# Kernel optimization log

Measured on AMD Instinct MI355X. Metric: run time of the kernel, lower is better.

The kernel has to match this reference:

```python
import jax, jax.numpy as jnp
import numpy as np

DILATION = 6
KS = 3
N = KS * KS  # 9 kernel sample points
PAD = 1      # zero padding inside DeformConv2d
EPS = 1e-5


def conv2d(x, w, b=None, padding=0):
    out = jax.lax.conv_general_dilated(
        x, w, window_strides=(1, 1),
        padding=[(padding, padding), (padding, padding)],
        dimension_numbers=('NCHW', 'OIHW', 'NCHW'))
    if b is not None:
        out = out + b[None, :, None, None]
    return out


def batchnorm_train(x, gamma, beta):
    # training-mode BN (module default): batch statistics over (N,H,W)
    mean = x.mean(axis=(0, 2, 3), keepdims=True)
    var = x.var(axis=(0, 2, 3), keepdims=True)
    return gamma[None, :, None, None] * (x - mean) * jax.lax.rsqrt(var + EPS) + beta[None, :, None, None]


def deform_conv(x, p_w, p_b, m_w, m_b, d_w, d_b, w):
    b, c, h, wd = x.shape
    offset = conv2d(x, p_w, p_b, padding=1)                 # (b, 2N, h, w)
    m = jax.nn.sigmoid(conv2d(x, m_w, m_b, padding=1))      # (b, N, h, w) modulation
    s = 2.0 * jax.nn.sigmoid(conv2d(x, d_w, d_b, padding=1))  # (b,1,h,w) adaptive dilation scale (=1 at logit 0)
    xp = jnp.pad(x, ((0, 0), (0, 0), (PAD, PAD), (PAD, PAD)))
    Hp, Wp = h + 2 * PAD, wd + 2 * PAD
    # kernel grid p_n, row-major (kh, kw) to match conv weight layout
    rng = jnp.arange(-(KS - 1) // 2, (KS - 1) // 2 + 1, dtype=x.dtype)
    pn_x, pn_y = jnp.meshgrid(rng, rng, indexing='ij')
    pn_x, pn_y = pn_x.reshape(-1), pn_y.reshape(-1)          # (N,)
    # base sampling positions (offset by PAD into padded map)
    p0_x = jnp.arange(1, h + 1, dtype=x.dtype)[:, None, None]    # (h,1,1)
    p0_y = jnp.arange(1, wd + 1, dtype=x.dtype)[None, :, None]   # (1,w,1)
    off = offset.transpose(0, 2, 3, 1)   # (b,h,w,2N)
    s_ = s.transpose(0, 2, 3, 1)         # (b,h,w,1)
    px = p0_x + DILATION * s_ * pn_x + off[..., :N]   # (b,h,w,N)
    py = p0_y + DILATION * s_ * pn_y + off[..., N:]
    fx, fy = jnp.floor(px), jnp.floor(py)
    qx_lt = jnp.clip(fx, 0, Hp - 1).astype(jnp.int32)
    qy_lt = jnp.clip(fy, 0, Wp - 1).astype(jnp.int32)
    qx_rb = jnp.clip(fx + 1, 0, Hp - 1).astype(jnp.int32)
    qy_rb = jnp.clip(fy + 1, 0, Wp - 1).astype(jnp.int32)
    pxc = jnp.clip(px, 0, Hp - 1)
    pyc = jnp.clip(py, 0, Wp - 1)
    g_lt = (1 + (qx_lt - pxc)) * (1 + (qy_lt - pyc))
    g_rb = (1 - (qx_rb - pxc)) * (1 - (qy_rb - pyc))
    g_lb = (1 + (qx_lt - pxc)) * (1 - (qy_rb - pyc))
    g_rt = (1 - (qx_rb - pxc)) * (1 + (qy_lt - pyc))

    def gather(qx, qy):
        idx = (qx * Wp + qy).reshape(b, 1, -1)                    # (b,1,h*w*N)
        xf = xp.reshape(b, c, Hp * Wp)
        out = jnp.take_along_axis(xf, jnp.broadcast_to(idx, (b, c, idx.shape[-1])), axis=2)
        return out.reshape(b, c, h, wd, N)

    x_off = (g_lt[:, None] * gather(qx_lt, qy_lt)
             + g_rb[:, None] * gather(qx_rb, qy_rb)
             + g_lb[:, None] * gather(qx_lt, qy_rb)
             + g_rt[:, None] * gather(qx_rb, qy_lt))
    x_off = x_off * m.transpose(0, 2, 3, 1)[:, None]              # modulation
    # final 3x3 conv over gathered samples == contraction over (c, N)
    return jnp.einsum('bchwn,ocn->bohw', x_off, w.reshape(w.shape[0], c, N))


def setup_inputs() -> dict:
    key = jax.random.key(0)
    ks = jax.random.split(key, 12)
    cin, c1, c2 = 512, 256, 64
    b, h, w = 2, 96, 96
    def rn(k, shape, scale):
        return jax.random.normal(k, shape, dtype=jnp.float32) * scale
    return {
        'x': rn(ks[0], (b, cin, h, w), 1.0),
        'bn1_g': jnp.ones((cin,), jnp.float32),
        'bn1_b': jnp.zeros((cin,), jnp.float32),
        'conv1_w': rn(ks[1], (c1, cin, 1, 1), (1.0 / cin) ** 0.5),
        'conv1_b': jnp.zeros((c1,), jnp.float32),
        'bn2_g': jnp.ones((c1,), jnp.float32),
        'bn2_b': jnp.zeros((c1,), jnp.float32),
        'p_w': rn(ks[2], (2 * N, c1, 3, 3), 0.01),
        'p_b': jnp.zeros((2 * N,), jnp.float32),
        'm_w': rn(ks[3], (N, c1, 3, 3), 0.01),
        'm_b': jnp.zeros((N,), jnp.float32),
        'd_w': rn(ks[4], (1, c1, 3, 3), 0.01),
        'd_b': jnp.zeros((1,), jnp.float32),
        'dconv_w': rn(ks[5], (c2, c1, 3, 3), (1.0 / (c1 * 9)) ** 0.5),
    }


def reference(x, bn1_g, bn1_b, conv1_w, conv1_b, bn2_g, bn2_b,
              p_w, p_b, m_w, m_b, d_w, d_b, dconv_w):
    f = jax.nn.relu(batchnorm_train(x, bn1_g, bn1_b))
    f = conv2d(f, conv1_w, conv1_b)
    f = batchnorm_train(f, bn2_g, bn2_b)
    return deform_conv(f, p_w, p_b, m_w, m_b, d_w, d_b, dconv_w)
```

## Files before the change

kernel.cpp:

```cpp
#include <hip/hip_runtime.h>
#include <hip/hip_bf16.h>
#include <math.h>

#define BATCH 2
#define CIN 512
#define C1 256
#define C2 64
#define HH 96
#define WW 96
#define HWSZ 9216
#define NPIX 18432
#define HP 98
#define WP 98

typedef __attribute__((ext_vector_type(8))) short bf16x8;
typedef __attribute__((ext_vector_type(4))) short bf16x4;
typedef __attribute__((ext_vector_type(4))) float f32x4;
typedef __attribute__((ext_vector_type(4))) unsigned int u32x4;
typedef __attribute__((ext_vector_type(2))) unsigned int u32x2;
typedef unsigned short u16;
typedef unsigned int u32;

__device__ __forceinline__ float bfu2f(u16 u) {
  u32 v = ((u32)u) << 16; return __builtin_bit_cast(float, v);
}
__device__ __forceinline__ u16 f2bfu(float f) {
  return __builtin_bit_cast(u16, __float2bfloat16(f));
}
__device__ __forceinline__ float rd_any(const void* p, size_t i, int fl) {
  return fl ? bfu2f(((const u16*)p)[i]) : ((const float*)p)[i];
}
__device__ __forceinline__ int get_fl(const u32* g1raw) {
  return g1raw[0] != 0x3F800000u;
}
__device__ __forceinline__ bf16x8 lds_frag(const u16* p) {
  bf16x4 lo = *(const bf16x4*)p;
  bf16x4 hi = *(const bf16x4*)(p + 4);
  bf16x8 r;
  r[0] = lo[0]; r[1] = lo[1]; r[2] = lo[2]; r[3] = lo[3];
  r[4] = hi[0]; r[5] = hi[1]; r[6] = hi[2]; r[7] = hi[3];
  return r;
}
__device__ __forceinline__ void split4(const f32x4& v, u32x2& ph, u32x2& pl) {
  u16 h0 = f2bfu(v[0]), h1 = f2bfu(v[1]), h2 = f2bfu(v[2]), h3 = f2bfu(v[3]);
  u16 l0 = f2bfu(v[0] - bfu2f(h0)), l1 = f2bfu(v[1] - bfu2f(h1));
  u16 l2 = f2bfu(v[2] - bfu2f(h2)), l3 = f2bfu(v[3] - bfu2f(h3));
  ph = (u32x2){(u32)h0 | ((u32)h1 << 16), (u32)h2 | ((u32)h3 << 16)};
  pl = (u32x2){(u32)l0 | ((u32)l1 << 16), (u32)l2 | ((u32)l3 << 16)};
}

__global__ __launch_bounds__(256) void prep_kernel(
    const void* cw, const void* pw, const void* mw, const void* dw, const void* dcw,
    const void* cb, const void* g1, const void* b1, const void* g2, const void* b2,
    const void* pb, const void* mb, const void* db,
    u16* __restrict__ W1b, u16* __restrict__ W1l,
    u16* __restrict__ Wofa, u16* __restrict__ Wofal,
    u16* __restrict__ Wab, u16* __restrict__ Wabl,
    float* __restrict__ canon, float* __restrict__ statz) {
  int e = blockIdx.x * 256 + threadIdx.x;
  if (e >= 356380) return;
  int fl = get_fl((const u32*)g1);
  if (e < 131072) {
    float v = rd_any(cw, e, fl);
    u16 h = f2bfu(v);
    W1b[e] = h; W1l[e] = f2bfu(v - bfu2f(h));
  } else if (e < 204800) {
    int i = e - 131072;
    int tap = i >> 13; int r = i & 8191; int m = r >> 8; int c = r & 255;
    float v = 0.f;
    if (m < 18)       v = rd_any(pw, (size_t)(m * 256 + c) * 9 + tap, fl);
    else if (m < 27)  v = rd_any(mw, (size_t)((m - 18) * 256 + c) * 9 + tap, fl);
    else if (m == 27) v = rd_any(dw, (size_t)c * 9 + tap, fl);
    u16 h = f2bfu(v);
    Wofa[i] = h; Wofal[i] = f2bfu(v - bfu2f(h));
  } else if (e < 352256) {
    int i = e - 204800;
    int n = i >> 14; int r = i & 16383; int o = r >> 8; int c = r & 255;
    float v = rd_any(dcw, (size_t)(o * 256 + c) * 9 + n, fl);
    u16 h = f2bfu(v);
    Wab[i] = h; Wabl[i] = f2bfu(v - bfu2f(h));
  } else if (e < 354076) {
    int i = e - 352256;
    const void* src; int off;
    if      (i < 256)  { src = cb; off = i; }
    else if (i < 768)  { src = g1; off = i - 256; }
    else if (i < 1280) { src = b1; off = i - 768; }
    else if (i < 1536) { src = g2; off = i - 1280; }
    else if (i < 1792) { src = b2; off = i - 1536; }
    else if (i < 1810) { src = pb; off = i - 1792; }
    else if (i < 1819) { src = mb; off = i - 1810; }
    else               { src = db; off = i - 1819; }
    canon[i] = rd_any(src, off, fl);
  } else {
    statz[e - 354076] = 0.f;
  }
}

__global__ __launch_bounds__(256) void bn_stats_kernel(
    const void* __restrict__ x, const float* __restrict__ gamma,
    const float* __restrict__ beta, float* __restrict__ scale,
    float* __restrict__ shift, float* __restrict__ sums, float* __restrict__ sumsq,
    int* __restrict__ cnt, const u32* __restrict__ g1raw, int force, int C) {
  int c = blockIdx.x, part = blockIdx.y, tid = threadIdx.x;
  int fl = force ? 1 : get_fl(g1raw);
  int b = part >> 1, half = part & 1;
  size_t base = ((size_t)(b * C + c)) * HWSZ + half * (HWSZ / 2);
  float s = 0.f, q = 0.f;
  if (fl) {
    const u16* p = (const u16*)x + base;
    for (int i = tid; i < 576; i += 256) {
      u32x4 U = *(const u32x4*)(p + i * 8);
      #pragma unroll
      for (int k = 0; k < 4; ++k) {
        float v0 = bfu2f((u16)(U[k] & 0xffff));
        float v1 = bfu2f((u16)(U[k] >> 16));
        s += v0 + v1; q = fmaf(v0, v0, fmaf(v1, v1, q));
      }
    }
  } else {
    const float* p = (const float*)x + base;
    for (int i = tid; i < 1152; i += 256) {
      f32x4 v = *(const f32x4*)(p + i * 4);
      #pragma unroll
      for (int k = 0; k < 4; ++k) { s += v[k]; q = fmaf(v[k], v[k], q); }
    }
  }
  __shared__ float sh[512];
  sh[tid] = s; sh[tid + 256] = q;
  __syncthreads();
  for (int off = 128; off > 0; off >>= 1) {
    if (tid < off) { sh[tid] += sh[tid + off]; sh[tid + 256] += sh[tid + 256 + off]; }
    __syncthreads();
  }
  if (tid == 0) {
    atomicAdd(&sums[c], sh[0]);
    atomicAdd(&sumsq[c], sh[256]);
    __threadfence();
    int old = atomicAdd(&cnt[c], 1);
    if (old == 3) {
      float S = atomicAdd(&sums[c], 0.f);
      float Q = atomicAdd(&sumsq[c], 0.f);
      float mean = S * (1.f / (float)NPIX);
      float var  = fmaxf(Q * (1.f / (float)NPIX) - mean * mean, 0.f);
      float sc = gamma[c] * rsqrtf(var + 1e-5f);
      scale[c] = sc;
      shift[c] = beta[c] - mean * sc;
    }
  }
}

__global__ __launch_bounds__(256) void conv1x1_kernel(
    const void* __restrict__ x, const u16* __restrict__ W1b, const u16* __restrict__ W1l,
    const float* __restrict__ cb, const float* __restrict__ scale,
    const float* __restrict__ shift, const u32* __restrict__ g1raw,
    u16* __restrict__ f1) {
  __shared__ u16 Bh[64][68];
  __shared__ u16 Bl[64][68];
  int tid = threadIdx.x;
  int fl = get_fl(g1raw);
  int bxr = blockIdx.x;
  int bx = (bxr & 7) * 36 + (bxr >> 3);
  int p0 = bx * 64;
  int co0 = blockIdx.y * 128;
  int b = p0 / HWSZ;
  int hw0 = p0 % HWSZ;
  int lane = tid & 63, wv = tid >> 6, quad = lane >> 4, mr = lane & 15;
  int m0 = co0 + wv * 32;
  f32x4 acc[2][4];
  #pragma unroll
  for (int i = 0; i < 2; ++i)
    #pragma unroll
    for (int j = 0; j < 4; ++j) acc[i][j] = (f32x4){0.f, 0.f, 0.f, 0.f};

  int spx = tid & 63, cg = tid >> 6;
  int gpx = hw0 + spx;
  for (int c0 = 0; c0 < CIN; c0 += 64) {
    __syncthreads();
    #pragma unroll
    for (int j = 0; j < 8; ++j) {
      int ci = c0 + cg * 16 + j * 2;
      float v0, v1;
      if (fl) {
        const u16* xb = (const u16*)x;
        v0 = bfu2f(xb[((size_t)(b * CIN + ci)) * HWSZ + gpx]);
        v1 = bfu2f(xb[((size_t)(b * CIN + ci + 1)) * HWSZ + gpx]);
      } else {
        const float* xf = (const float*)x;
        v0 = xf[((size_t)(b * CIN + ci)) * HWSZ + gpx];
        v1 = xf[((size_t)(b * CIN + ci + 1)) * HWSZ + gpx];
      }
      v0 = fmaxf(fmaf(v0, scale[ci], shift[ci]), 0.f);
      v1 = fmaxf(fmaf(v1, scale[ci + 1], shift[ci + 1]), 0.f);
      u16 h0 = f2bfu(v0), h1 = f2bfu(v1);
      u16 l0 = f2bfu(v0 - bfu2f(h0)), l1 = f2bfu(v1 - bfu2f(h1));
      *(u32*)&Bh[spx][cg * 16 + j * 2] = (u32)h0 | ((u32)h1 << 16);
      *(u32*)&Bl[spx][cg * 16 + j * 2] = (u32)l0 | ((u32)l1 << 16);
    }
    __syncthreads();
    #pragma unroll
    for (int kk2 = 0; kk2 < 2; ++kk2) {
      int kk = kk2 * 32;
      #pragma unroll
      for (int mf = 0; mf < 2; ++mf) {
        size_t wix = (size_t)(m0 + mf * 16 + mr) * CIN + c0 + kk + quad * 8;
        bf16x8 ah = *(const bf16x8*)(W1b + wix);
        bf16x8 al = *(const bf16x8*)(W1l + wix);
        #pragma unroll
        for (int nt = 0; nt < 4; ++nt) {
          bf16x8 bl = lds_frag(&Bl[nt * 16 + mr][kk + quad * 8]);
          bf16x8 bh = lds_frag(&Bh[nt * 16 + mr][kk + quad * 8]);
          acc[mf][nt] = __builtin_amdgcn_mfma_f32_16x16x32_bf16(ah, bl, acc[mf][nt], 0, 0, 0);
          acc[mf][nt] = __builtin_amdgcn_mfma_f32_16x16x32_bf16(al, bh, acc[mf][nt], 0, 0, 0);
          acc[mf][nt] = __builtin_amdgcn_mfma_f32_16x16x32_bf16(ah, bh, acc[mf][nt], 0, 0, 0);
        }
      }
    }
  }
  #pragma unroll
  for (int mf = 0; mf < 2; ++mf) {
    #pragma unroll
    for (int nt = 0; nt < 4; ++nt) {
      #pragma unroll
      for (int r = 0; r < 4; ++r) {
        int co = m0 + mf * 16 + quad * 4 + r;
        f1[((size_t)(b * C1 + co)) * HWSZ + hw0 + nt * 16 + mr] = f2bfu(acc[mf][nt][r] + cb[co]);
      }
    }
  }
}

__global__ __launch_bounds__(256) void bn2pad_kernel(
    const u16* __restrict__ f1, const float* __restrict__ scale,
    const float* __restrict__ shift, float* __restrict__ xpf) {
  int bid = blockIdx.x;
  int ht = bid % 144; int ct = (bid / 144) & 3; int b = bid / 576;
  int hw0 = ht * 64, c0 = ct * 64;
  __shared__ float t[64][65];
  int tid = threadIdx.x;
  #pragma unroll
  for (int it = 0; it < 16; ++it) {
    int e = it * 256 + tid;
    int p = e & 63, ci = e >> 6;
    float v = bfu2f(f1[((size_t)(b * C1 + c0 + ci)) * HWSZ + hw0 + p]);
    t[ci][p] = fmaf(v, scale[c0 + ci], shift[c0 + ci]);
  }
  __syncthreads();
  #pragma unroll
  for (int it = 0; it < 16; ++it) {
    int e = it * 256 + tid;
    int ci = e & 63, p = e >> 6;
    int hw = hw0 + p; int h = hw / WW; int w = hw % WW;
    xpf[(((size_t)(b * HP) + h + 1) * WP + w + 1) * C1 + c0 + ci] = t[ci][p];
  }
}

__global__ __launch_bounds__(256) void init_kernel(
    const u32* __restrict__ g1raw, void* __restrict__ outv,
    float* __restrict__ oscr, float* __restrict__ opart, float* __restrict__ xpf) {
  int i = blockIdx.x * 256 + threadIdx.x;
  if (i < 1179648) {
    if (get_fl(g1raw)) { ((u16*)outv)[i] = 0; oscr[i] = 0.f; }
    else               { ((float*)outv)[i] = 0.f; }
  } else if (i < 1769472) {
    opart[i - 1179648] = 0.f;
  } else {
    int k = i - 1769472;
    int ch = k & 255; int pxi = k >> 8;
    int bb = pxi / 388; int r = pxi % 388;
    int h, w;
    if (r < 98)      { h = 0;  w = r; }
    else if (r < 196){ h = 97; w = r - 98; }
    else if (r < 292){ h = r - 196 + 1; w = 0; }
    else             { h = r - 292 + 1; w = 97; }
    xpf[(((size_t)(bb * HP) + h) * WP + w) * C1 + ch] = 0.f;
  }
}

__global__ __launch_bounds__(256) void offconv_kernel(
    const float* __restrict__ xpf, const u16* __restrict__ Wofa, const u16* __restrict__ Wofal,
    const float* __restrict__ pbc, const float* __restrict__ mbc,
    const float* __restrict__ dbc, float* __restrict__ opart) {
  __shared__ u16 Vh[32][68];
  __shared__ u16 Vl[32][68];
  int tid = threadIdx.x;
  int bxr = blockIdx.x;
  int bx = (bxr & 7) * 72 + (bxr >> 3);
  int tg = blockIdx.y;
  int p0 = bx * 32;
  int b = p0 / HWSZ;
  int hw = p0 % HWSZ; int h0 = hw / WW; int w0 = hw % WW;
  int lane = tid & 63, wv = tid >> 6, quad = lane >> 4, mr = lane & 15;
  int m0 = (wv & 1) * 16;
  int ntile = wv >> 1;
  int srow = tid >> 4;
  int scol = (tid & 15) * 4;
  f32x4 acc = (f32x4){0.f, 0.f, 0.f, 0.f};
  for (int tt = 0; tt < 3; ++tt) {
    int tap = tg * 3 + tt;
    int th = tap / 3, tw = tap % 3;
    const float* base = xpf + ((size_t)(b * HP + h0 + th) * WP + (w0 + tw)) * C1;
    for (int c0i = 0; c0i < 4; ++c0i) {
      int c0 = c0i * 64;
      if (tt | c0i) __syncthreads();
      #pragma unroll
      for (int pass = 0; pass < 2; ++pass) {
        int px = pass * 16 + srow;
        f32x4 v = *(const f32x4*)(base + (size_t)px * C1 + c0 + scol);
        u32x2 ph, pl;
        split4(v, ph, pl);
        *(u32x2*)&Vh[px][scol] = ph;
        *(u32x2*)&Vl[px][scol] = pl;
      }
      __syncthreads();
      #pragma unroll
      for (int kk2 = 0; kk2 < 2; ++kk2) {
        int kof = kk2 * 32 + quad * 8;
        size_t wix = (size_t)(tap * 32 + m0 + mr) * C1 + c0 + kof;
        bf16x8 ah = *(const bf16x8*)(Wofa + wix);
        bf16x8 al = *(const bf16x8*)(Wofal + wix);
        bf16x8 bl = lds_frag(&Vl[ntile * 16 + mr][kof]);
        bf16x8 bh = lds_frag(&Vh[ntile * 16 + mr][kof]);
        acc = __builtin_amdgcn_mfma_f32_16x16x32_bf16(ah, bl, acc, 0, 0, 0);
        acc = __builtin_amdgcn_mfma_f32_16x16x32_bf16(al, bh, acc, 0, 0, 0);
        acc = __builtin_amdgcn_mfma_f32_16x16x32_bf16(ah, bh, acc, 0, 0, 0);
      }
    }
  }
  int px = ntile * 16 + mr;
  #pragma unroll
  for (int r = 0; r < 4; ++r) {
    int m = m0 + quad * 4 + r;
    if (m < 28) {
      float v = acc[r];
      if (tg == 0) v += (m < 18) ? pbc[m] : ((m < 27) ? mbc[m - 18] : dbc[0]);
      atomicAdd(&opart[(size_t)m * NPIX + p0 + px], v);
    }
  }
}

__global__ __launch_bounds__(256) void deform_kernel(
    const float* __restrict__ xpf, const u16* __restrict__ Wab, const u16* __restrict__ Wabl,
    const float* __restrict__ opart, const u32* __restrict__ g1raw,
    float* __restrict__ oscr, void* __restrict__ outv) {
  __shared__ u16   Vh[64][68];
  __shared__ u16   Vl[64][68];
  __shared__ int   smi[4][64];
  __shared__ float smw[4][64];
  int tid = threadIdx.x;
  int bxr = blockIdx.x;
  int bx = (bxr & 7) * 36 + (bxr >> 3);
  int n = blockIdx.y;
  int p0 = bx * 64;
  int b = p0 / HWSZ;
  int hw0 = p0 % HWSZ;

  if (tid < 64) {
    int p = tid;
    int bp = p0 + p;
    int hw = hw0 + p; int h = hw / WW; int w = hw % WW;
    float offx = opart[(size_t)n * NPIX + bp];
    float offy = opart[(size_t)(9 + n) * NPIX + bp];
    float mlog = opart[(size_t)(18 + n) * NPIX + bp];
    float slog = opart[(size_t)27 * NPIX + bp];
    float mm = 1.f / (1.f + expf(-mlog));
    float s  = 2.f / (1.f + expf(-slog));
    float pnx = (float)(n / 3 - 1), pny = (float)(n % 3 - 1);
    float px = (float)(h + 1) + 6.f * s * pnx + offx;
    float py = (float)(w + 1) + 6.f * s * pny + offy;
    float fx = floorf(px), fy = floorf(py);
    float qxlt = fminf(fmaxf(fx, 0.f), 97.f);
    float qylt = fminf(fmaxf(fy, 0.f), 97.f);
    float qxrb = fminf(fmaxf(fx + 1.f, 0.f), 97.f);
    float qyrb = fminf(fmaxf(fy + 1.f, 0.f), 97.f);
    float pxc = fminf(fmaxf(px, 0.f), 97.f);
    float pyc = fminf(fmaxf(py, 0.f), 97.f);
    float glt = (1.f + (qxlt - pxc)) * (1.f + (qylt - pyc));
    float grb = (1.f - (qxrb - pxc)) * (1.f - (qyrb - pyc));
    float glb = (1.f + (qxlt - pxc)) * (1.f - (qyrb - pyc));
    float grt = (1.f - (qxrb - pxc)) * (1.f + (qylt - pyc));
    int ixlt = (int)qxlt, iylt = (int)qylt, ixrb = (int)qxrb, iyrb = (int)qyrb;
    int base = b * (HP * WP);
    smi[0][p] = base + ixlt * WP + iylt;  smw[0][p] = glt * mm;
    smi[1][p] = base + ixrb * WP + iyrb;  smw[1][p] = grb * mm;
    smi[2][p] = base + ixlt * WP + iyrb;  smw[2][p] = glb * mm;
    smi[3][p] = base + ixrb * WP + iylt;  smw[3][p] = grt * mm;
  }
  __syncthreads();

  int lane = tid & 63, wv = tid >> 6, quad = lane >> 4, mr = lane & 15;
  int m0 = wv * 16;
  int srow = tid >> 4;
  int scol = (tid & 15) * 4;
  f32x4 acc[4];
  #pragma unroll
  for (int i = 0; i < 4; ++i) acc[i] = (f32x4){0.f, 0.f, 0.f, 0.f};

  for (int c0i = 0; c0i < 4; ++c0i) {
    int c0 = c0i * 64;
    if (c0i) __syncthreads();
    #pragma unroll
    for (int pass = 0; pass < 4; ++pass) {
      int px = pass * 16 + srow;
      const float* r0 = xpf + (size_t)smi[0][px] * C1 + c0 + scol;
      const float* r1 = xpf + (size_t)smi[1][px] * C1 + c0 + scol;
      const float* r2 = xpf + (size_t)smi[2][px] * C1 + c0 + scol;
      const float* r3 = xpf + (size_t)smi[3][px] * C1 + c0 + scol;
      float w0 = smw[0][px], w1 = smw[1][px], w2 = smw[2][px], w3 = smw[3][px];
      f32x4 v0 = *(const f32x4*)r0;
      f32x4 v1 = *(const f32x4*)r1;
      f32x4 v2 = *(const f32x4*)r2;
      f32x4 v3 = *(const f32x4*)r3;
      f32x4 vc;
      #pragma unroll
      for (int j = 0; j < 4; ++j)
        vc[j] = fmaf(w0, v0[j], fmaf(w1, v1[j], fmaf(w2, v2[j], w3 * v3[j])));
      u32x2 ph, pl;
      split4(vc, ph, pl);
      *(u32x2*)&Vh[px][scol] = ph;
      *(u32x2*)&Vl[px][scol] = pl;
    }
    __syncthreads();
    #pragma unroll
    for (int kk2 = 0; kk2 < 2; ++kk2) {
      int kof = kk2 * 32 + quad * 8;
      size_t wix = (size_t)(n * C2 + m0 + mr) * C1 + c0 + kof;
      bf16x8 ah = *(const bf16x8*)(Wab + wix);
      bf16x8 al = *(const bf16x8*)(Wabl + wix);
      #pragma unroll
      for (int nt = 0; nt < 4; ++nt) {
        bf16x8 bl = lds_frag(&Vl[nt * 16 + mr][kof]);
        bf16x8 bh = lds_frag(&Vh[nt * 16 + mr][kof]);
        acc[nt] = __builtin_amdgcn_mfma_f32_16x16x32_bf16(ah, bl, acc[nt], 0, 0, 0);
        acc[nt] = __builtin_amdgcn_mfma_f32_16x16x32_bf16(al, bh, acc[nt], 0, 0, 0);
        acc[nt] = __builtin_amdgcn_mfma_f32_16x16x32_bf16(ah, bh, acc[nt], 0, 0, 0);
      }
    }
  }
  int fl = get_fl(g1raw);
  float* tgt = fl ? oscr : (float*)outv;
  #pragma unroll
  for (int nt = 0; nt < 4; ++nt) {
    #pragma unroll
    for (int r = 0; r < 4; ++r) {
      int o = m0 + quad * 4 + r;
      int hw = hw0 + nt * 16 + mr;
      atomicAdd(&tgt[((size_t)(b * C2 + o)) * HWSZ + hw], acc[nt][r]);
    }
  }
}

__global__ void cvt_out_kernel(const u32* __restrict__ g1raw,
                               const float* __restrict__ oscr, void* __restrict__ outv) {
  if (!get_fl(g1raw)) return;
  int i = blockIdx.x * 256 + threadIdx.x;
  ((u16*)outv)[i] = f2bfu(oscr[i]);
}

extern "C" void kernel_launch(void* const* d_in, const int* in_sizes, int n_in,
                              void* d_out, int out_size, void* d_ws, size_t ws_size,
                              hipStream_t stream) {
  const void* x       = d_in[0];
  const void* bn1_g   = d_in[1];
  const void* bn1_b   = d_in[2];
  const void* conv1_w = d_in[3];
  const void* conv1_b = d_in[4];
  const void* bn2_g   = d_in[5];
  const void* bn2_b   = d_in[6];
  const void* p_w     = d_in[7];
  const void* p_b     = d_in[8];
  const void* m_w     = d_in[9];
  const void* m_b     = d_in[10];
  const void* d_w     = d_in[11];
  const void* d_b     = d_in[12];
  const void* dconv_w = d_in[13];
  const u32* g1raw = (const u32*)bn1_g;

  float* ws = (float*)d_ws;
  float* canon = ws + 16;
  float* cbc = canon + 0;
  float* g1c = canon + 256;
  float* b1c = canon + 768;
  float* g2c = canon + 1280;
  float* b2c = canon + 1536;
  float* pbc = canon + 1792;
  float* mbc = canon + 1810;
  float* dbc = canon + 1819;
  float* scale1 = ws + 1840;
  float* shift1 = ws + 2352;
  float* scale2 = ws + 2864;
  float* shift2 = ws + 3120;
  float* statz  = ws + 3376;
  float* sums1  = statz;
  float* sumsq1 = statz + 512;
  int*   cnt1   = (int*)(statz + 1024);
  float* sums2  = statz + 1536;
  float* sumsq2 = statz + 1792;
  int*   cnt2   = (int*)(statz + 2048);
  u16* W1b   = (u16*)(ws + 5680);
  u16* W1l   = (u16*)(ws + 71216);
  u16* Wofa  = (u16*)(ws + 136752);
  u16* Wofal = (u16*)(ws + 173616);
  u16* Wab   = (u16*)(ws + 210480);
  u16* Wabl  = (u16*)(ws + 284208);
  u16* f1    = (u16*)(ws + 357936);
  float* oscr  = ws + 357936;
  float* opart = ws + 1537584;
  float* xpf   = ws + 2717232;

  prep_kernel<<<1393, 256, 0, stream>>>(conv1_w, p_w, m_w, d_w, dconv_w,
                                        conv1_b, bn1_g, bn1_b, bn2_g, bn2_b,
                                        p_b, m_b, d_b,
                                        W1b, W1l, Wofa, Wofal, Wab, Wabl, canon, statz);
  bn_stats_kernel<<<dim3(CIN, 4), 256, 0, stream>>>(x, g1c, b1c, scale1, shift1,
                                                    sums1, sumsq1, cnt1, g1raw, 0, CIN);
  conv1x1_kernel<<<dim3(288, 2), 256, 0, stream>>>(x, W1b, W1l, cbc, scale1, shift1, g1raw, f1);
  bn_stats_kernel<<<dim3(C1, 4), 256, 0, stream>>>(f1, g2c, b2c, scale2, shift2,
                                                   sums2, sumsq2, cnt2, g1raw, 1, C1);
  bn2pad_kernel<<<1152, 256, 0, stream>>>(f1, scale2, shift2, xpf);
  init_kernel<<<7688, 256, 0, stream>>>(g1raw, d_out, oscr, opart, xpf);
  offconv_kernel<<<dim3(576, 3), 256, 0, stream>>>(xpf, Wofa, Wofal, pbc, mbc, dbc, opart);
  deform_kernel<<<dim3(288, 9), 256, 0, stream>>>(xpf, Wab, Wabl, opart, g1raw, oscr, d_out);
  cvt_out_kernel<<<4608, 256, 0, stream>>>(g1raw, oscr, d_out);
}
```

Baseline: 320.2 us.

## Fuse BN2 stats into conv1x1, merge zero-init into prep, prefetch deform gathers

The 1x1 conv kernel now covers all 256 output channels per block and accumulates BN2 sums and sums of squares through warp shuffles and atomics. This removes the separate BN2 stats pass over f1, and bn2pad now derives scale and shift from those sums. When the workspace is large enough, zero-initialisation of outputs, partial buffers and padding borders moves into the prep kernel, which drops a launch. The deform kernel also software-prefetches the next channel chunk's bilinear gather loads into registers while the MFMAs run. In exchange, register pressure rises in the conv1x1 and deform kernels, and the conv1x1 grid shrinks to 288 blocks.

```diff
diff --git a/kernel.cpp b/kernel.cpp
--- a/kernel.cpp
+++ b/kernel.cpp
@@ -49,6 +49,11 @@
   pl = (u32x2){(u32)l0 | ((u32)l1 << 16), (u32)l2 | ((u32)l3 << 16)};
 }
 
+#define PREP_BASE 356380
+#define NOPART 589824
+#define NOUT 1179648
+#define NBORD 198656
+
 __global__ __launch_bounds__(256) void prep_kernel(
     const void* cw, const void* pw, const void* mw, const void* dw, const void* dcw,
     const void* cb, const void* g1, const void* b1, const void* g2, const void* b2,
@@ -56,9 +61,11 @@
     u16* __restrict__ W1b, u16* __restrict__ W1l,
     u16* __restrict__ Wofa, u16* __restrict__ Wofal,
     u16* __restrict__ Wab, u16* __restrict__ Wabl,
-    float* __restrict__ canon, float* __restrict__ statz) {
+    float* __restrict__ canon, float* __restrict__ statz,
+    float* __restrict__ opartZ, float* __restrict__ oscrZ, void* __restrict__ outZ,
+    float* __restrict__ xpfB, int nextra) {
   int e = blockIdx.x * 256 + threadIdx.x;
-  if (e >= 356380) return;
+  if (e >= PREP_BASE + nextra) return;
   int fl = get_fl((const u32*)g1);
   if (e < 131072) {
     float v = rd_any(cw, e, fl);
@@ -91,8 +98,49 @@
     else if (i < 1819) { src = mb; off = i - 1810; }
     else               { src = db; off = i - 1819; }
     canon[i] = rd_any(src, off, fl);
+  } else if (e < PREP_BASE) {
+    statz[e - 354076] = 0.f;
   } else {
-    statz[e - 354076] = 0.f;
+    int k = e - PREP_BASE;
+    if (k < NOPART) {
+      opartZ[k] = 0.f;
+    } else if (k < NOPART + NOUT) {
+      int i = k - NOPART;
+      if (fl) { ((u16*)outZ)[i] = 0; oscrZ[i] = 0.f; }
+      else    { ((float*)outZ)[i] = 0.f; }
+    } else {
+      int i = k - NOPART - NOUT;
+      int ch = i & 255; int pxi = i >> 8;
+      int bb = pxi / 388; int r = pxi % 388;
+      int h, w;
+      if (r < 98)      { h = 0;  w = r; }
+      else if (r < 196){ h = 97; w = r - 98; }
+      else if (r < 292){ h = r - 196 + 1; w = 0; }
+      else             { h = r - 292 + 1; w = 97; }
+      xpfB[(((size_t)(bb * HP) + h) * WP + w) * C1 + ch] = 0.f;
+    }
+  }
+}
+
+__global__ __launch_bounds__(256) void init_kernel(
+    const u32* __restrict__ g1raw, void* __restrict__ outv,
+    float* __restrict__ oscr, float* __restrict__ opart, float* __restrict__ xpf) {
+  int i = blockIdx.x * 256 + threadIdx.x;
+  if (i < NOUT) {
+    if (get_fl(g1raw)) { ((u16*)outv)[i] = 0; oscr[i] = 0.f; }
+    else               { ((float*)outv)[i] = 0.f; }
+  } else if (i < NOUT + NOPART) {
+    opart[i - NOUT] = 0.f;
+  } else {
+    int k = i - NOUT - NOPART;
+    int ch = k & 255; int pxi = k >> 8;
+    int bb = pxi / 388; int r = pxi % 388;
+    int h, w;
+    if (r < 98)      { h = 0;  w = r; }
+    else if (r < 196){ h = 97; w = r - 98; }
+    else if (r < 292){ h = r - 196 + 1; w = 0; }
+    else             { h = r - 292 + 1; w = 97; }
+    xpf[(((size_t)(bb * HP) + h) * WP + w) * C1 + ch] = 0.f;
   }
 }
 
@@ -100,9 +148,9 @@
     const void* __restrict__ x, const float* __restrict__ gamma,
     const float* __restrict__ beta, float* __restrict__ scale,
     float* __restrict__ shift, float* __restrict__ sums, float* __restrict__ sumsq,
-    int* __restrict__ cnt, const u32* __restrict__ g1raw, int force, int C) {
+    int* __restrict__ cnt, const u32* __restrict__ g1raw, int C) {
   int c = blockIdx.x, part = blockIdx.y, tid = threadIdx.x;
-  int fl = force ? 1 : get_fl(g1raw);
+  int fl = get_fl(g1raw);
   int b = part >> 1, half = part & 1;
   size_t base = ((size_t)(b * C + c)) * HWSZ + half * (HWSZ / 2);
   float s = 0.f, q = 0.f;
@@ -153,7 +201,7 @@
     const void* __restrict__ x, const u16* __restrict__ W1b, const u16* __restrict__ W1l,
     const float* __restrict__ cb, const float* __restrict__ scale,
     const float* __restrict__ shift, const u32* __restrict__ g1raw,
-    u16* __restrict__ f1) {
+    u16* __restrict__ f1, float* __restrict__ sums2, float* __restrict__ sumsq2) {
   __shared__ u16 Bh[64][68];
   __shared__ u16 Bl[64][68];
   int tid = threadIdx.x;
@@ -161,14 +209,13 @@
   int bxr = blockIdx.x;
   int bx = (bxr & 7) * 36 + (bxr >> 3);
   int p0 = bx * 64;
-  int co0 = blockIdx.y * 128;
   int b = p0 / HWSZ;
   int hw0 = p0 % HWSZ;
   int lane = tid & 63, wv = tid >> 6, quad = lane >> 4, mr = lane & 15;
-  int m0 = co0 + wv * 32;
-  f32x4 acc[2][4];
-  #pragma unroll
-  for (int i = 0; i < 2; ++i)
+  int m0 = wv * 64;
+  f32x4 acc[4][4];
+  #pragma unroll
+  for (int i = 0; i < 4; ++i)
     #pragma unroll
     for (int j = 0; j < 4; ++j) acc[i][j] = (f32x4){0.f, 0.f, 0.f, 0.f};
 
@@ -201,7 +248,7 @@
     for (int kk2 = 0; kk2 < 2; ++kk2) {
       int kk = kk2 * 32;
       #pragma unroll
-      for (int mf = 0; mf < 2; ++mf) {
+      for (int mf = 0; mf < 4; ++mf) {
         size_t wix = (size_t)(m0 + mf * 16 + mr) * CIN + c0 + kk + quad * 8;
         bf16x8 ah = *(const bf16x8*)(W1b + wix);
         bf16x8 al = *(const bf16x8*)(W1l + wix);
@@ -217,32 +264,57 @@
     }
   }
   #pragma unroll
-  for (int mf = 0; mf < 2; ++mf) {
-    #pragma unroll
-    for (int nt = 0; nt < 4; ++nt) {
-      #pragma unroll
-      for (int r = 0; r < 4; ++r) {
-        int co = m0 + mf * 16 + quad * 4 + r;
-        f1[((size_t)(b * C1 + co)) * HWSZ + hw0 + nt * 16 + mr] = f2bfu(acc[mf][nt][r] + cb[co]);
+  for (int mf = 0; mf < 4; ++mf) {
+    #pragma unroll
+    for (int r = 0; r < 4; ++r) {
+      int co = m0 + mf * 16 + quad * 4 + r;
+      float bi = cb[co];
+      float sv = 0.f, sq = 0.f;
+      #pragma unroll
+      for (int nt = 0; nt < 4; ++nt) {
+        float v = acc[mf][nt][r] + bi;
+        f1[((size_t)(b * C1 + co)) * HWSZ + hw0 + nt * 16 + mr] = f2bfu(v);
+        sv += v; sq = fmaf(v, v, sq);
+      }
+      #pragma unroll
+      for (int m = 1; m < 16; m <<= 1) {
+        sv += __shfl_xor(sv, m);
+        sq += __shfl_xor(sq, m);
+      }
+      if (mr == 0) {
+        atomicAdd(&sums2[co], sv);
+        atomicAdd(&sumsq2[co], sq);
       }
     }
   }
 }
 
 __global__ __launch_bounds__(256) void bn2pad_kernel(
-    const u16* __restrict__ f1, const float* __restrict__ scale,
-    const float* __restrict__ shift, float* __restrict__ xpf) {
+    const u16* __restrict__ f1, const float* __restrict__ sums2,
+    const float* __restrict__ sumsq2, const float* __restrict__ g2c,
+    const float* __restrict__ b2c, float* __restrict__ xpf) {
   int bid = blockIdx.x;
   int ht = bid % 144; int ct = (bid / 144) & 3; int b = bid / 576;
   int hw0 = ht * 64, c0 = ct * 64;
   __shared__ float t[64][65];
+  __shared__ float s2[64], sh2[64];
   int tid = threadIdx.x;
+  if (tid < 64) {
+    int c = c0 + tid;
+    float S = sums2[c], Q = sumsq2[c];
+    float mean = S * (1.f / (float)NPIX);
+    float var  = fmaxf(Q * (1.f / (float)NPIX) - mean * mean, 0.f);
+    float sc = g2c[c] * rsqrtf(var + 1e-5f);
+    s2[tid] = sc;
+    sh2[tid] = b2c[c] - mean * sc;
+  }
+  __syncthreads();
   #pragma unroll
   for (int it = 0; it < 16; ++it) {
     int e = it * 256 + tid;
     int p = e & 63, ci = e >> 6;
     float v = bfu2f(f1[((size_t)(b * C1 + c0 + ci)) * HWSZ + hw0 + p]);
-    t[ci][p] = fmaf(v, scale[c0 + ci], shift[c0 + ci]);
+    t[ci][p] = fmaf(v, s2[ci], sh2[ci]);
   }
   __syncthreads();
   #pragma unroll
@@ -251,28 +323,6 @@
     int ci = e & 63, p = e >> 6;
     int hw = hw0 + p; int h = hw / WW; int w = hw % WW;
     xpf[(((size_t)(b * HP) + h + 1) * WP + w + 1) * C1 + c0 + ci] = t[ci][p];
-  }
-}
-
-__global__ __launch_bounds__(256) void init_kernel(
-    const u32* __restrict__ g1raw, void* __restrict__ outv,
-    float* __restrict__ oscr, float* __restrict__ opart, float* __restrict__ xpf) {
-  int i = blockIdx.x * 256 + threadIdx.x;
-  if (i < 1179648) {
-    if (get_fl(g1raw)) { ((u16*)outv)[i] = 0; oscr[i] = 0.f; }
-    else               { ((float*)outv)[i] = 0.f; }
-  } else if (i < 1769472) {
-    opart[i - 1179648] = 0.f;
-  } else {
-    int k = i - 1769472;
-    int ch = k & 255; int pxi = k >> 8;
-    int bb = pxi / 388; int r = pxi % 388;
-    int h, w;
-    if (r < 98)      { h = 0;  w = r; }
-    else if (r < 196){ h = 97; w = r - 98; }
-    else if (r < 292){ h = r - 196 + 1; w = 0; }
-    else             { h = r - 292 + 1; w = 97; }
-    xpf[(((size_t)(bb * HP) + h) * WP + w) * C1 + ch] = 0.f;
   }
 }
 
@@ -395,31 +445,48 @@
   #pragma unroll
   for (int i = 0; i < 4; ++i) acc[i] = (f32x4){0.f, 0.f, 0.f, 0.f};
 
+  const float* bp[4][4];
+  float wt[4][4];
+  #pragma unroll
+  for (int pass = 0; pass < 4; ++pass) {
+    int px = pass * 16 + srow;
+    #pragma unroll
+    for (int c = 0; c < 4; ++c) {
+      bp[pass][c] = xpf + (size_t)smi[c][px] * C1 + scol;
+      wt[pass][c] = smw[c][px];
+    }
+  }
+  f32x4 pv[4][4];
+  #pragma unroll
+  for (int pass = 0; pass < 4; ++pass)
+    #pragma unroll
+    for (int c = 0; c < 4; ++c) pv[pass][c] = *(const f32x4*)(bp[pass][c]);
+
   for (int c0i = 0; c0i < 4; ++c0i) {
     int c0 = c0i * 64;
     if (c0i) __syncthreads();
     #pragma unroll
     for (int pass = 0; pass < 4; ++pass) {
       int px = pass * 16 + srow;
-      const float* r0 = xpf + (size_t)smi[0][px] * C1 + c0 + scol;
-      const float* r1 = xpf + (size_t)smi[1][px] * C1 + c0 + scol;
-      const float* r2 = xpf + (size_t)smi[2][px] * C1 + c0 + scol;
-      const float* r3 = xpf + (size_t)smi[3][px] * C1 + c0 + scol;
-      float w0 = smw[0][px], w1 = smw[1][px], w2 = smw[2][px], w3 = smw[3][px];
-      f32x4 v0 = *(const f32x4*)r0;
-      f32x4 v1 = *(const f32x4*)r1;
-      f32x4 v2 = *(const f32x4*)r2;
-      f32x4 v3 = *(const f32x4*)r3;
       f32x4 vc;
       #pragma unroll
       for (int j = 0; j < 4; ++j)
-        vc[j] = fmaf(w0, v0[j], fmaf(w1, v1[j], fmaf(w2, v2[j], w3 * v3[j])));
+        vc[j] = fmaf(wt[pass][0], pv[pass][0][j],
+                 fmaf(wt[pass][1], pv[pass][1][j],
+                  fmaf(wt[pass][2], pv[pass][2][j], wt[pass][3] * pv[pass][3][j])));
       u32x2 ph, pl;
       split4(vc, ph, pl);
       *(u32x2*)&Vh[px][scol] = ph;
       *(u32x2*)&Vl[px][scol] = pl;
     }
     __syncthreads();
+    if (c0i < 3) {
+      int cn = c0 + 64;
+      #pragma unroll
+      for (int pass = 0; pass < 4; ++pass)
+        #pragma unroll
+        for (int c = 0; c < 4; ++c) pv[pass][c] = *(const f32x4*)(bp[pass][c] + cn);
+    }
     #pragma unroll
     for (int kk2 = 0; kk2 < 2; ++kk2) {
       int kof = kk2 * 32 + quad * 8;
@@ -487,15 +554,12 @@
   float* dbc = canon + 1819;
   float* scale1 = ws + 1840;
   float* shift1 = ws + 2352;
-  float* scale2 = ws + 2864;
-  float* shift2 = ws + 3120;
   float* statz  = ws + 3376;
   float* sums1  = statz;
   float* sumsq1 = statz + 512;
   int*   cnt1   = (int*)(statz + 1024);
   float* sums2  = statz + 1536;
   float* sumsq2 = statz + 1792;
-  int*   cnt2   = (int*)(statz + 2048);
   u16* W1b   = (u16*)(ws + 5680);
   u16* W1l   = (u16*)(ws + 71216);
   u16* Wofa  = (u16*)(ws + 136752);
@@ -503,21 +567,32 @@
   u16* Wab   = (u16*)(ws + 210480);
   u16* Wabl  = (u16*)(ws + 284208);
   u16* f1    = (u16*)(ws + 357936);
-  float* oscr  = ws + 357936;
-  float* opart = ws + 1537584;
-  float* xpf   = ws + 2717232;
-
-  prep_kernel<<<1393, 256, 0, stream>>>(conv1_w, p_w, m_w, d_w, dconv_w,
-                                        conv1_b, bn1_g, bn1_b, bn2_g, bn2_b,
-                                        p_b, m_b, d_b,
-                                        W1b, W1l, Wofa, Wofal, Wab, Wabl, canon, statz);
+
+  bool bigws = ws_size >= (size_t)9403952 * 4 + 64;
+  float *opart, *oscr, *xpf;
+  if (bigws) {
+    opart = ws + 2717232;
+    oscr  = ws + 3307056;
+    xpf   = ws + 4486704;
+  } else {
+    oscr  = ws + 357936;
+    opart = ws + 1537584;
+    xpf   = ws + 2717232;
+  }
+
+  prep_kernel<<<bigws ? 9081 : 1393, 256, 0, stream>>>(
+      conv1_w, p_w, m_w, d_w, dconv_w,
+      conv1_b, bn1_g, bn1_b, bn2_g, bn2_b, p_b, m_b, d_b,
+      W1b, W1l, Wofa, Wofal, Wab, Wabl, canon, statz,
+      opart, oscr, d_out, xpf, bigws ? (NOPART + NOUT + NBORD) : 0);
   bn_stats_kernel<<<dim3(CIN, 4), 256, 0, stream>>>(x, g1c, b1c, scale1, shift1,
-                                                    sums1, sumsq1, cnt1, g1raw, 0, CIN);
-  conv1x1_kernel<<<dim3(288, 2), 256, 0, stream>>>(x, W1b, W1l, cbc, scale1, shift1, g1raw, f1);
-  bn_stats_kernel<<<dim3(C1, 4), 256, 0, stream>>>(f1, g2c, b2c, scale2, shift2,
-                                                   sums2, sumsq2, cnt2, g1raw, 1, C1);
-  bn2pad_kernel<<<1152, 256, 0, stream>>>(f1, scale2, shift2, xpf);
-  init_kernel<<<7688, 256, 0, stream>>>(g1raw, d_out, oscr, opart, xpf);
+                                                    sums1, sumsq1, cnt1, g1raw, CIN);
+  conv1x1_kernel<<<288, 256, 0, stream>>>(x, W1b, W1l, cbc, scale1, shift1, g1raw,
+                                          f1, sums2, sumsq2);
+  bn2pad_kernel<<<1152, 256, 0, stream>>>(f1, sums2, sumsq2, g2c, b2c, xpf);
+  if (!bigws)
+    init_kernel<<<(NOUT + NOPART + NBORD + 255) / 256, 256, 0, stream>>>(
+        g1raw, d_out, oscr, opart, xpf);
   offconv_kernel<<<dim3(576, 3), 256, 0, stream>>>(xpf, Wofa, Wofal, pbc, mbc, dbc, opart);
   deform_kernel<<<dim3(288, 9), 256, 0, stream>>>(xpf, Wab, Wabl, opart, g1raw, oscr, d_out);
   cvt_out_kernel<<<4608, 256, 0, stream>>>(g1raw, oscr, d_out);
```

Result: slower. 339.0 us (+5.9%).
